# Optimization experiments

Measured on AMD Instinct MI355X. Metric: run time of the kernel, lower is better.

Reference implementation:

```python
import jax, jax.numpy as jnp
import numpy as np

DIM = 64
N_NODES = 20000
N_EDGES = 50000
N_GRAPHS = 256
CONV_STEPS = 12
S2S_STEPS = 3


def leaky(v):
    return jnp.where(v > 0, v, 0.01 * v)


def setup_inputs() -> dict:
    key = jax.random.key(0)
    ks = jax.random.split(key, 24)
    gn = lambda k, shape, s=0.1: jax.random.normal(k, shape, dtype=jnp.float32) * s
    return {
        "x": gn(ks[0], (N_NODES, 72), 1.0),
        "edge_attr": gn(ks[1], (N_EDGES, 4), 1.0),
        "edge_index": jax.random.randint(ks[2], (2, N_EDGES), 0, N_NODES),
        "batch": jnp.sort(jax.random.randint(ks[3], (N_NODES,), 0, N_GRAPHS)),
        "lin0_w": gn(ks[4], (DIM, 72)),
        "lin0_b": gn(ks[5], (DIM,)),
        "net_w1": gn(ks[6], (128, 4)),
        "net_b1": gn(ks[7], (128,)),
        "net_w2": gn(ks[8], (DIM * DIM, 128), 0.02),
        "net_b2": gn(ks[9], (DIM * DIM,), 0.02),
        "root_w": gn(ks[10], (DIM, DIM)),
        "conv_b": gn(ks[11], (DIM,)),
        "gru_w_ih": gn(ks[12], (3 * DIM, DIM)),
        "gru_w_hh": gn(ks[13], (3 * DIM, DIM)),
        "gru_b_ih": gn(ks[14], (3 * DIM,)),
        "gru_b_hh": gn(ks[15], (3 * DIM,)),
        "lstm_w_ih": gn(ks[16], (4 * DIM, 2 * DIM)),
        "lstm_w_hh": gn(ks[17], (4 * DIM, DIM)),
        "lstm_b_ih": gn(ks[18], (4 * DIM,)),
        "lstm_b_hh": gn(ks[19], (4 * DIM,)),
        "lin3_w": gn(ks[20], (1, 2 * DIM)),
        "lin3_b": gn(ks[21], (1,)),
    }


def _forward(x, edge_attr, lin0_w, lin0_b, net_w1, net_b1, net_w2, net_b2,
             root_w, conv_b, gru_w_ih, gru_w_hh, gru_b_ih, gru_b_hh,
             lstm_w_ih, lstm_w_hh, lstm_b_ih, lstm_b_hh, lin3_w, lin3_b,
             edge_index, batch):
    src, dst = edge_index[0], edge_index[1]
    out = leaky(x @ lin0_w.T + lin0_b)  # [N, D]
    h = out
    # Edge-conditioned weights (same every conv step -> compute once): [E, D, D]
    w_e = (leaky(edge_attr @ net_w1.T + net_b1) @ net_w2.T + net_b2).reshape(N_EDGES, DIM, DIM)
    deg = jnp.clip(jax.ops.segment_sum(jnp.ones((N_EDGES,), jnp.float32), dst,
                                       num_segments=N_NODES), 1.0)[:, None]
    for _ in range(CONV_STEPS):
        # NNConv: gather src feats, per-edge matmul, scatter-mean to dst, + root + bias
        msg = jnp.einsum('ei,eio->eo', out[src], w_e)  # [E, D]
        agg = jax.ops.segment_sum(msg, dst, num_segments=N_NODES) / deg
        m = leaky(agg + out @ root_w + conv_b)
        # GRU cell (seq_len=1)
        gi = m @ gru_w_ih.T + gru_b_ih
        gh = h @ gru_w_hh.T + gru_b_hh
        i_r, i_z, i_n = jnp.split(gi, 3, axis=-1)
        h_r, h_z, h_n = jnp.split(gh, 3, axis=-1)
        r = jax.nn.sigmoid(i_r + h_r)
        z = jax.nn.sigmoid(i_z + h_z)
        n = jnp.tanh(i_n + r * h_n)
        h = (1.0 - z) * n + z * h
        out = h
    # Set2Set pooling over graphs
    q_star = jnp.zeros((N_GRAPHS, 2 * DIM), jnp.float32)
    hl = jnp.zeros((N_GRAPHS, DIM), jnp.float32)
    cl = jnp.zeros((N_GRAPHS, DIM), jnp.float32)
    for _ in range(S2S_STEPS):
        gates = q_star @ lstm_w_ih.T + lstm_b_ih + hl @ lstm_w_hh.T + lstm_b_hh
        g_i, g_f, g_g, g_o = jnp.split(gates, 4, axis=-1)
        cl = jax.nn.sigmoid(g_f) * cl + jax.nn.sigmoid(g_i) * jnp.tanh(g_g)
        hl = jax.nn.sigmoid(g_o) * jnp.tanh(cl)
        q = hl  # [B, D]
        e = jnp.sum(out * q[batch], axis=-1)  # [N]
        e_max = jax.ops.segment_max(e, batch, num_segments=N_GRAPHS)
        a = jnp.exp(e - e_max[batch])
        a = a / (jax.ops.segment_sum(a, batch, num_segments=N_GRAPHS)[batch] + 1e-16)
        r_read = jax.ops.segment_sum(a[:, None] * out, batch, num_segments=N_GRAPHS)
        q_star = jnp.concatenate([q, r_read], axis=-1)  # [B, 2D]
    return q_star @ lin3_w.T + lin3_b  # [B, 1]


def reference(x, edge_attr, edge_index, batch, lin0_w, lin0_b, net_w1, net_b1,
              net_w2, net_b2, root_w, conv_b, gru_w_ih, gru_w_hh, gru_b_ih,
              gru_b_hh, lstm_w_ih, lstm_w_hh, lstm_b_ih, lstm_b_hh, lin3_w, lin3_b):
    return _forward(x, edge_attr, lin0_w, lin0_b, net_w1, net_b1, net_w2, net_b2,
                    root_w, conv_b, gru_w_ih, gru_w_hh, gru_b_ih, gru_b_hh,
                    lstm_w_ih, lstm_w_hh, lstm_b_ih, lstm_b_hh, lin3_w, lin3_b,
                    edge_index, batch)
```

## Files before the change

kernel.cpp:

```cpp
#include <hip/hip_runtime.h>

#define DIM 64
#define NN 20000
#define NE 50000
#define NG 256
#define CONV_STEPS 12
#define S2S 3

typedef float floatx4 __attribute__((ext_vector_type(4)));
typedef short short8 __attribute__((ext_vector_type(8)));

__device__ __forceinline__ unsigned short f2bf(float f) {
    unsigned u = __float_as_uint(f);
    unsigned r = (u + 0x7fffu + ((u >> 16) & 1u)) >> 16;
    return (unsigned short)r;
}
__device__ __forceinline__ float sigmoidf(float x) { return 1.f / (1.f + __expf(-x)); }
__device__ __forceinline__ float tanh_fast(float x) {
    float ax = fabsf(x);
    float t = __expf(-2.f * ax);
    float r = (1.f - t) / (1.f + t);
    return copysignf(r, x);
}
__device__ __forceinline__ float leaky(float v) { return v > 0.f ? v : 0.01f * v; }

__global__ __launch_bounds__(256) void prep_kernel(const float* __restrict__ w2,
        const float* __restrict__ wih, const float* __restrict__ whh,
        unsigned short* __restrict__ w2bf, float* __restrict__ wihT, float* __restrict__ whhT) {
    int idx = blockIdx.x * 256 + threadIdx.x;
    const int W2N = 4096 * 128, GT = 192 * 64;
    if (idx < W2N) {
        w2bf[idx] = f2bf(w2[idx]);
    } else if (idx < W2N + GT) {
        int t = idx - W2N; int j = t / 64, i = t % 64;
        wihT[i * 192 + j] = wih[t];
    } else if (idx < W2N + 2 * GT) {
        int t = idx - W2N - GT; int j = t / 64, i = t % 64;
        whhT[i * 192 + j] = whh[t];
    }
}

__global__ __launch_bounds__(256) void h1_kernel(const float* __restrict__ ea,
        const float* __restrict__ w1, const float* __restrict__ b1, unsigned short* __restrict__ h1) {
    int idx = blockIdx.x * 256 + threadIdx.x;
    if (idx >= NE * 128) return;
    int e = idx >> 7, k = idx & 127;
    const float* a = ea + (size_t)e * 4;
    const float* w = w1 + (size_t)k * 4;
    float acc = b1[k] + a[0] * w[0] + a[1] * w[1] + a[2] * w[2] + a[3] * w[3];
    h1[idx] = f2bf(leaky(acc));
}

__global__ __launch_bounds__(256) void lin0_kernel(const float* __restrict__ x,
        const float* __restrict__ w, const float* __restrict__ b, float* __restrict__ X) {
    int gid = blockIdx.x * 256 + threadIdx.x;
    int n = gid >> 6, o = gid & 63;
    if (n >= NN) return;
    float acc = b[o];
    const float* xr = x + (size_t)n * 72;
    const float* wr = w + (size_t)o * 72;
    #pragma unroll 8
    for (int i = 0; i < 72; ++i) acc += xr[i] * wr[i];
    X[(size_t)n * 64 + o] = leaky(acc);
}

__global__ __launch_bounds__(256) void deg_kernel(const int* __restrict__ ei, float* __restrict__ deg) {
    int e = blockIdx.x * 256 + threadIdx.x;
    if (e < NE) atomicAdd(&deg[ei[NE + e]], 1.f);
}

__global__ void gstart_kernel(const int* __restrict__ batch, int* __restrict__ gstart) {
    int g = blockIdx.x * blockDim.x + threadIdx.x;
    if (g > NG) return;
    int lo = 0, hi = NN;
    while (lo < hi) { int mid = (lo + hi) >> 1; if (batch[mid] < g) lo = mid + 1; else hi = mid; }
    gstart[g] = lo;
}

__device__ __forceinline__ void stage_w2(const unsigned short* __restrict__ w2, int ib,
                                         unsigned short* buf, int wv, int lane) {
    #pragma unroll
    for (int i = 0; i < 4; ++i) {
        int d0 = (i * 4 + wv) * 1024;
        int d = d0 + lane * 16;
        int rowl = d >> 8;
        int cb = d & 255;
        int srcb = rowl * 256 + (cb ^ ((rowl & 7) << 4));
        const char* g = (const char*)w2 + (size_t)ib * 16384 + srcb;
        __builtin_amdgcn_global_load_lds(
            (const __attribute__((address_space(1))) void*)g,
            (__attribute__((address_space(3))) void*)((char*)buf + d0),
            16, 0, 0);
    }
}

__global__ __launch_bounds__(256) void edge_msg_fused(
        const unsigned short* __restrict__ h1,
        const unsigned short* __restrict__ w2,
        const float* __restrict__ b2,
        const float* __restrict__ X,
        const int* __restrict__ ei, float* __restrict__ agg) {
    __shared__ float xs_t[32 * 128];
    __shared__ unsigned short w2buf[2][8192];
    int tid = threadIdx.x;
    int e0b = blockIdx.x * 128;
    int ibBase = blockIdx.y * 32;

    {
        int e_l = tid & 127, half = tid >> 7;
        int e = e0b + e_l; if (e >= NE) e = NE - 1;
        int src = ei[e];
        const float4* xr = (const float4*)(X + (size_t)src * 64 + ibBase + half * 16);
        #pragma unroll
        for (int c = 0; c < 4; ++c) {
            float4 v = xr[c];
            int f = half * 16 + c * 4;
            xs_t[(f + 0) * 128 + e_l] = v.x;
            xs_t[(f + 1) * 128 + e_l] = v.y;
            xs_t[(f + 2) * 128 + e_l] = v.z;
            xs_t[(f + 3) * 128 + e_l] = v.w;
        }
    }

    int wv = tid >> 6, lane = tid & 63;
    int row = lane & 15, kq = lane >> 4;
    int e0w = e0b + wv * 32;

    short8 afr[2][4];
    #pragma unroll
    for (int mt = 0; mt < 2; ++mt) {
        int e = e0w + mt * 16 + row; if (e >= NE) e = NE - 1;
        const short8* ap = (const short8*)(h1 + (size_t)e * 128 + kq * 8);
        #pragma unroll
        for (int kc = 0; kc < 4; ++kc) afr[mt][kc] = ap[kc * 4];
    }

    stage_w2(w2, ibBase, w2buf[0], wv, lane);
    __syncthreads();

    floatx4 msg[2][4];
    #pragma unroll
    for (int mt = 0; mt < 2; ++mt)
        #pragma unroll
        for (int ot = 0; ot < 4; ++ot) msg[mt][ot] = (floatx4){0.f, 0.f, 0.f, 0.f};

    for (int il = 0; il < 32; ++il) {
        int cur = il & 1;
        if (il < 31) stage_w2(w2, ibBase + il + 1, w2buf[cur ^ 1], wv, lane);
        int ib = ibBase + il;
        float4 xv[2];
        #pragma unroll
        for (int mt = 0; mt < 2; ++mt)
            xv[mt] = *(const float4*)&xs_t[il * 128 + wv * 32 + mt * 16 + kq * 4];
        #pragma unroll
        for (int ot = 0; ot < 4; ++ot) {
            int row_l = ot * 16 + row;
            const char* bbase = (const char*)w2buf[cur] + row_l * 256;
            int sw = (row_l & 7) << 4;
            short8 bf0 = *(const short8*)(bbase + ((kq * 16      ) ^ sw));
            short8 bf1 = *(const short8*)(bbase + ((kq * 16 +  64) ^ sw));
            short8 bf2 = *(const short8*)(bbase + ((kq * 16 + 128) ^ sw));
            short8 bf3 = *(const short8*)(bbase + ((kq * 16 + 192) ^ sw));
            float bias = b2[ib * 64 + row_l];
            #pragma unroll
            for (int mt = 0; mt < 2; ++mt) {
                floatx4 acc = {0.f, 0.f, 0.f, 0.f};
                acc = __builtin_amdgcn_mfma_f32_16x16x32_bf16(afr[mt][0], bf0, acc, 0, 0, 0);
                acc = __builtin_amdgcn_mfma_f32_16x16x32_bf16(afr[mt][1], bf1, acc, 0, 0, 0);
                acc = __builtin_amdgcn_mfma_f32_16x16x32_bf16(afr[mt][2], bf2, acc, 0, 0, 0);
                acc = __builtin_amdgcn_mfma_f32_16x16x32_bf16(afr[mt][3], bf3, acc, 0, 0, 0);
                float xm0 = xv[mt].x, xm1 = xv[mt].y, xm2 = xv[mt].z, xm3 = xv[mt].w;
                msg[mt][ot][0] += xm0 * (acc[0] + bias);
                msg[mt][ot][1] += xm1 * (acc[1] + bias);
                msg[mt][ot][2] += xm2 * (acc[2] + bias);
                msg[mt][ot][3] += xm3 * (acc[3] + bias);
            }
        }
        __syncthreads();
    }

    #pragma unroll
    for (int mt = 0; mt < 2; ++mt) {
        #pragma unroll
        for (int r = 0; r < 4; ++r) {
            int e = e0w + mt * 16 + kq * 4 + r;
            if (e < NE) {
                int dst = ei[NE + e];
                #pragma unroll
                for (int ot = 0; ot < 4; ++ot)
                    atomicAdd(&agg[(size_t)dst * 64 + ot * 16 + row], msg[mt][ot][r]);
            }
        }
    }
}

__global__ __launch_bounds__(256) void node_update(float* __restrict__ X, float* __restrict__ agg,
        const float* __restrict__ deg, const float* __restrict__ root_w, const float* __restrict__ conv_b,
        const float* __restrict__ wihT, const float* __restrict__ whhT,
        const float* __restrict__ bih, const float* __restrict__ bhh) {
    int gid = blockIdx.x * 256 + threadIdx.x;
    int wv = gid >> 6, lane = gid & 63;
    int n0 = wv * 4;
    if (n0 >= NN) return;
    float xv[4], m[4];
    #pragma unroll
    for (int t = 0; t < 4; ++t) xv[t] = X[(size_t)(n0 + t) * 64 + lane];
    float cb = conv_b[lane];
    #pragma unroll
    for (int t = 0; t < 4; ++t) {
        size_t id = (size_t)(n0 + t) * 64 + lane;
        float a = agg[id]; agg[id] = 0.f;
        m[t] = a / fmaxf(deg[n0 + t], 1.f) + cb;
    }
    #pragma unroll 8
    for (int i = 0; i < 64; ++i) {
        float rw = root_w[i * 64 + lane];
        #pragma unroll
        for (int t = 0; t < 4; ++t) m[t] += __shfl(xv[t], i) * rw;
    }
    #pragma unroll
    for (int t = 0; t < 4; ++t) m[t] = leaky(m[t]);
    float g0[4], g1[4], g2[4], h0[4], h1g[4], h2[4];
    float bi0 = bih[lane], bi1 = bih[64 + lane], bi2 = bih[128 + lane];
    float bh0 = bhh[lane], bh1 = bhh[64 + lane], bh2 = bhh[128 + lane];
    #pragma unroll
    for (int t = 0; t < 4; ++t) { g0[t] = bi0; g1[t] = bi1; g2[t] = bi2; h0[t] = bh0; h1g[t] = bh1; h2[t] = bh2; }
    #pragma unroll 8
    for (int i = 0; i < 64; ++i) {
        float wi0 = wihT[i * 192 + lane], wi1 = wihT[i * 192 + 64 + lane], wi2 = wihT[i * 192 + 128 + lane];
        float wh0 = whhT[i * 192 + lane], wh1 = whhT[i * 192 + 64 + lane], wh2 = whhT[i * 192 + 128 + lane];
        #pragma unroll
        for (int t = 0; t < 4; ++t) {
            float mb = __shfl(m[t], i), hb = __shfl(xv[t], i);
            g0[t] += mb * wi0; g1[t] += mb * wi1; g2[t] += mb * wi2;
            h0[t] += hb * wh0; h1g[t] += hb * wh1; h2[t] += hb * wh2;
        }
    }
    #pragma unroll
    for (int t = 0; t < 4; ++t) {
        float r = sigmoidf(g0[t] + h0[t]);
        float z = sigmoidf(g1[t] + h1g[t]);
        float nn = tanh_fast(g2[t] + r * h2[t]);
        X[(size_t)(n0 + t) * 64 + lane] = (1.f - z) * nn + z * xv[t];
    }
}

__global__ __launch_bounds__(256) void lstm_kernel(const float* __restrict__ qstar,
        float* __restrict__ hl, float* __restrict__ cl,
        const float* __restrict__ wih, const float* __restrict__ whh,
        const float* __restrict__ bih, const float* __restrict__ bhh) {
    int g = blockIdx.x, tid = threadIdx.x;
    __shared__ float qs[128], hs[64], gates[256];
    if (tid < 128) qs[tid] = qstar[(size_t)g * 128 + tid];
    else if (tid < 192) hs[tid - 128] = hl[(size_t)g * 64 + tid - 128];
    __syncthreads();
    float acc = bih[tid] + bhh[tid];
    const float* wr = wih + (size_t)tid * 128;
    #pragma unroll 8
    for (int k = 0; k < 128; ++k) acc += qs[k] * wr[k];
    const float* wr2 = whh + (size_t)tid * 64;
    #pragma unroll 8
    for (int k = 0; k < 64; ++k) acc += hs[k] * wr2[k];
    gates[tid] = acc;
    __syncthreads();
    if (tid < 64) {
        float gi = gates[tid], gf = gates[64 + tid], gg = gates[128 + tid], go = gates[192 + tid];
        float c = sigmoidf(gf) * cl[(size_t)g * 64 + tid] + sigmoidf(gi) * tanh_fast(gg);
        float h = sigmoidf(go) * tanh_fast(c);
        cl[(size_t)g * 64 + tid] = c;
        hl[(size_t)g * 64 + tid] = h;
    }
}

__global__ __launch_bounds__(256) void e_kernel(const float* __restrict__ X, const float* __restrict__ hl,
        const int* __restrict__ batch, float* __restrict__ ev) {
    int gid = blockIdx.x * 256 + threadIdx.x;
    int n = gid >> 6, lane = gid & 63;
    if (n >= NN) return;
    int g = batch[n];
    float v = X[(size_t)n * 64 + lane] * hl[(size_t)g * 64 + lane];
    #pragma unroll
    for (int m = 32; m >= 1; m >>= 1) v += __shfl_xor(v, m);
    if (lane == 0) ev[n] = v;
}

__global__ __launch_bounds__(256) void pool_kernel(const float* __restrict__ X, const float* __restrict__ ev,
        const float* __restrict__ hl, const int* __restrict__ gstart, float* __restrict__ qstar) {
    int g = blockIdx.x, tid = threadIdx.x;
    int s0 = gstart[g], s1 = gstart[g + 1];
    __shared__ float red[256];
    __shared__ float sh_max, sh_sum;
    float lm = -3.0e38f;
    for (int n = s0 + tid; n < s1; n += 256) lm = fmaxf(lm, ev[n]);
    red[tid] = lm; __syncthreads();
    for (int s = 128; s > 0; s >>= 1) { if (tid < s) red[tid] = fmaxf(red[tid], red[tid + s]); __syncthreads(); }
    if (tid == 0) sh_max = red[0];
    __syncthreads();
    float mx = sh_max;
    float ls = 0.f;
    for (int n = s0 + tid; n < s1; n += 256) ls += __expf(ev[n] - mx);
    __syncthreads();
    red[tid] = ls; __syncthreads();
    for (int s = 128; s > 0; s >>= 1) { if (tid < s) red[tid] += red[tid + s]; __syncthreads(); }
    if (tid == 0) sh_sum = red[0];
    __syncthreads();
    float inv = 1.f / (sh_sum + 1e-16f);
    int wv = tid >> 6, lane = tid & 63;
    float fa = 0.f;
    for (int n = s0 + wv; n < s1; n += 4) fa += __expf(ev[n] - mx) * inv * X[(size_t)n * 64 + lane];
    __syncthreads();
    red[tid] = fa; __syncthreads();
    if (tid < 64) {
        float r = red[tid] + red[64 + tid] + red[128 + tid] + red[192 + tid];
        qstar[(size_t)g * 128 + 64 + tid] = r;
        qstar[(size_t)g * 128 + tid] = hl[(size_t)g * 64 + tid];
    }
}

__global__ __launch_bounds__(256) void final_kernel(const float* __restrict__ qstar,
        const float* __restrict__ w3, const float* __restrict__ b3, float* __restrict__ out) {
    int gid = blockIdx.x * 256 + threadIdx.x;
    int g = gid >> 6, lane = gid & 63;
    if (g >= NG) return;
    float v = qstar[(size_t)g * 128 + lane] * w3[lane] + qstar[(size_t)g * 128 + 64 + lane] * w3[64 + lane];
    #pragma unroll
    for (int m = 32; m >= 1; m >>= 1) v += __shfl_xor(v, m);
    if (lane == 0) out[g] = v + b3[0];
}

extern "C" void kernel_launch(void* const* d_in, const int* in_sizes, int n_in,
                              void* d_out, int out_size, void* d_ws, size_t ws_size,
                              hipStream_t stream) {
    const float* x        = (const float*)d_in[0];
    const float* ea       = (const float*)d_in[1];
    const int*   ei       = (const int*)d_in[2];
    const int*   batch    = (const int*)d_in[3];
    const float* lin0_w   = (const float*)d_in[4];
    const float* lin0_b   = (const float*)d_in[5];
    const float* net_w1   = (const float*)d_in[6];
    const float* net_b1   = (const float*)d_in[7];
    const float* net_w2   = (const float*)d_in[8];
    const float* net_b2   = (const float*)d_in[9];
    const float* root_w   = (const float*)d_in[10];
    const float* conv_b   = (const float*)d_in[11];
    const float* gru_w_ih = (const float*)d_in[12];
    const float* gru_w_hh = (const float*)d_in[13];
    const float* gru_b_ih = (const float*)d_in[14];
    const float* gru_b_hh = (const float*)d_in[15];
    const float* lstm_w_ih= (const float*)d_in[16];
    const float* lstm_w_hh= (const float*)d_in[17];
    const float* lstm_b_ih= (const float*)d_in[18];
    const float* lstm_b_hh= (const float*)d_in[19];
    const float* lin3_w   = (const float*)d_in[20];
    const float* lin3_b   = (const float*)d_in[21];
    float* out = (float*)d_out;

    char* base = (char*)d_ws;
    size_t off = 0;
    auto alloc = [&](size_t b) { size_t o = off; off += (b + 255) & ~(size_t)255; return o; };
    size_t o_h1    = alloc((size_t)NE * 128 * 2);
    size_t o_X     = alloc((size_t)NN * 64 * 4);
    size_t o_agg   = alloc((size_t)NN * 64 * 4);
    size_t o_deg   = alloc((size_t)NN * 4);
    size_t o_ev    = alloc((size_t)NN * 4);
    size_t o_s2s   = alloc((size_t)(NG * 128 + NG * 64 + NG * 64) * 4);
    size_t o_gst   = alloc((size_t)(NG + 1) * 4);
    size_t o_w2bf  = alloc((size_t)4096 * 128 * 2);
    size_t o_wihT  = alloc((size_t)192 * 64 * 4);
    size_t o_whhT  = alloc((size_t)192 * 64 * 4);
    if (ws_size < off) return;

    unsigned short* h1   = (unsigned short*)(base + o_h1);
    float* X    = (float*)(base + o_X);
    float* agg  = (float*)(base + o_agg);
    float* deg  = (float*)(base + o_deg);
    float* ev   = (float*)(base + o_ev);
    float* qstar= (float*)(base + o_s2s);
    float* hl   = qstar + NG * 128;
    float* cl   = hl + NG * 64;
    int*   gst  = (int*)(base + o_gst);
    unsigned short* w2bf = (unsigned short*)(base + o_w2bf);
    float* wihT = (float*)(base + o_wihT);
    float* whhT = (float*)(base + o_whhT);

    hipMemsetAsync(deg, 0, (size_t)NN * 4, stream);
    hipMemsetAsync(agg, 0, (size_t)NN * 64 * 4, stream);
    hipMemsetAsync(qstar, 0, (size_t)(NG * 128 + NG * 64 + NG * 64) * 4, stream);

    prep_kernel<<<(4096 * 128 + 2 * 192 * 64 + 255) / 256, 256, 0, stream>>>(
        net_w2, gru_w_ih, gru_w_hh, w2bf, wihT, whhT);
    h1_kernel<<<(NE * 128 + 255) / 256, 256, 0, stream>>>(ea, net_w1, net_b1, h1);
    lin0_kernel<<<(NN * 64 + 255) / 256, 256, 0, stream>>>(x, lin0_w, lin0_b, X);
    deg_kernel<<<(NE + 255) / 256, 256, 0, stream>>>(ei, deg);
    gstart_kernel<<<2, 256, 0, stream>>>(batch, gst);

    const dim3 EGRID((NE + 127) / 128, 2);
    for (int s = 0; s < CONV_STEPS; ++s) {
        edge_msg_fused<<<EGRID, 256, 0, stream>>>(h1, w2bf, net_b2, X, ei, agg);
        node_update<<<(NN / 4 * 64 + 255) / 256, 256, 0, stream>>>(
            X, agg, deg, root_w, conv_b, wihT, whhT, gru_b_ih, gru_b_hh);
    }

    for (int s = 0; s < S2S; ++s) {
        lstm_kernel<<<NG, 256, 0, stream>>>(qstar, hl, cl, lstm_w_ih, lstm_w_hh, lstm_b_ih, lstm_b_hh);
        e_kernel<<<(NN * 64 + 255) / 256, 256, 0, stream>>>(X, hl, batch, ev);
        pool_kernel<<<NG, 256, 0, stream>>>(X, ev, hl, gst, qstar);
    }
    final_kernel<<<(NG * 64 + 255) / 256, 256, 0, stream>>>(qstar, lin3_w, lin3_b, out);
}
```

Before: 1.946 ms.

## Prefetch w2 two stages ahead with manual vmcnt waits and raw barriers

Result: faster. 1.888 ms (-3.0%).

```diff
diff --git a/kernel.cpp b/kernel.cpp
--- a/kernel.cpp
+++ b/kernel.cpp
@@ -135,8 +135,12 @@
         for (int kc = 0; kc < 4; ++kc) afr[mt][kc] = ap[kc * 4];
     }
 
-    stage_w2(w2, ibBase, w2buf[0], wv, lane);
-    __syncthreads();
+    __syncthreads();
+    stage_w2(w2, ibBase + 0, w2buf[0], wv, lane);
+    stage_w2(w2, ibBase + 1, w2buf[1], wv, lane);
+    asm volatile("s_waitcnt vmcnt(4)" ::: "memory");
+    __builtin_amdgcn_s_barrier();
+    __builtin_amdgcn_sched_barrier(0);
 
     floatx4 msg[2][4];
     #pragma unroll
@@ -146,7 +150,6 @@
 
     for (int il = 0; il < 32; ++il) {
         int cur = il & 1;
-        if (il < 31) stage_w2(w2, ibBase + il + 1, w2buf[cur ^ 1], wv, lane);
         int ib = ibBase + il;
         float4 xv[2];
         #pragma unroll
@@ -157,26 +160,37 @@
             int row_l = ot * 16 + row;
             const char* bbase = (const char*)w2buf[cur] + row_l * 256;
             int sw = (row_l & 7) << 4;
-            short8 bf0 = *(const short8*)(bbase + ((kq * 16      ) ^ sw));
-            short8 bf1 = *(const short8*)(bbase + ((kq * 16 +  64) ^ sw));
-            short8 bf2 = *(const short8*)(bbase + ((kq * 16 + 128) ^ sw));
-            short8 bf3 = *(const short8*)(bbase + ((kq * 16 + 192) ^ sw));
+            short8 b0 = *(const short8*)(bbase + ((kq * 16      ) ^ sw));
+            short8 b1 = *(const short8*)(bbase + ((kq * 16 +  64) ^ sw));
+            short8 b2f = *(const short8*)(bbase + ((kq * 16 + 128) ^ sw));
+            short8 b3 = *(const short8*)(bbase + ((kq * 16 + 192) ^ sw));
             float bias = b2[ib * 64 + row_l];
             #pragma unroll
             for (int mt = 0; mt < 2; ++mt) {
                 floatx4 acc = {0.f, 0.f, 0.f, 0.f};
-                acc = __builtin_amdgcn_mfma_f32_16x16x32_bf16(afr[mt][0], bf0, acc, 0, 0, 0);
-                acc = __builtin_amdgcn_mfma_f32_16x16x32_bf16(afr[mt][1], bf1, acc, 0, 0, 0);
-                acc = __builtin_amdgcn_mfma_f32_16x16x32_bf16(afr[mt][2], bf2, acc, 0, 0, 0);
-                acc = __builtin_amdgcn_mfma_f32_16x16x32_bf16(afr[mt][3], bf3, acc, 0, 0, 0);
-                float xm0 = xv[mt].x, xm1 = xv[mt].y, xm2 = xv[mt].z, xm3 = xv[mt].w;
-                msg[mt][ot][0] += xm0 * (acc[0] + bias);
-                msg[mt][ot][1] += xm1 * (acc[1] + bias);
-                msg[mt][ot][2] += xm2 * (acc[2] + bias);
-                msg[mt][ot][3] += xm3 * (acc[3] + bias);
+                acc = __builtin_amdgcn_mfma_f32_16x16x32_bf16(afr[mt][0], b0, acc, 0, 0, 0);
+                acc = __builtin_amdgcn_mfma_f32_16x16x32_bf16(afr[mt][1], b1, acc, 0, 0, 0);
+                acc = __builtin_amdgcn_mfma_f32_16x16x32_bf16(afr[mt][2], b2f, acc, 0, 0, 0);
+                acc = __builtin_amdgcn_mfma_f32_16x16x32_bf16(afr[mt][3], b3, acc, 0, 0, 0);
+                msg[mt][ot][0] += xv[mt].x * (acc[0] + bias);
+                msg[mt][ot][1] += xv[mt].y * (acc[1] + bias);
+                msg[mt][ot][2] += xv[mt].z * (acc[2] + bias);
+                msg[mt][ot][3] += xv[mt].w * (acc[3] + bias);
             }
         }
-        __syncthreads();
+        if (il < 31) {
+            __builtin_amdgcn_sched_barrier(0);
+            __builtin_amdgcn_s_barrier();
+            __builtin_amdgcn_sched_barrier(0);
+            if (il + 2 < 32) {
+                stage_w2(w2, ibBase + il + 2, w2buf[cur], wv, lane);
+                asm volatile("s_waitcnt vmcnt(4)" ::: "memory");
+            } else {
+                asm volatile("s_waitcnt vmcnt(0)" ::: "memory");
+            }
+            __builtin_amdgcn_s_barrier();
+            __builtin_amdgcn_sched_barrier(0);
+        }
     }
 
     #pragma unroll
```
